# Optimization experiments

Measured on AMD Instinct MI355X. Metric: run time of the kernel, lower is better.

## Reference

```python
import jax, jax.numpy as jnp
import numpy as np

NUM_ROUTES = 32
LN_EPS = 1e-5


def _ln(x, g, b):
    mu = jnp.mean(x, axis=-1, keepdims=True)
    var = jnp.mean(jnp.square(x - mu), axis=-1, keepdims=True)
    return (x - mu) * jax.lax.rsqrt(var + LN_EPS) * g + b


def setup_inputs() -> dict:
    key = jax.random.key(0)
    ks = jax.random.split(key, 16)
    B, N, D = 64, 512, 512
    s = 1.0 / np.sqrt(D)
    return {
        "tokens": jax.random.normal(ks[0], (B, N, D), jnp.float32),
        "token_mask": jax.random.bernoulli(ks[1], 0.7, (B, N)),
        "route_ids": jax.random.randint(ks[2], (N,), 0, NUM_ROUTES),
        # token_ffn: LayerNorm + Linear(D,4D) + GELU + Linear(4D,D)
        "ln1_g": jnp.ones((D,), jnp.float32),
        "ln1_b": jnp.zeros((D,), jnp.float32),
        "w1": jax.random.normal(ks[3], (D, 4 * D), jnp.float32) * s,
        "b1": jnp.zeros((4 * D,), jnp.float32),
        "w2": jax.random.normal(ks[4], (4 * D, D), jnp.float32) * (0.5 * s),
        "b2": jnp.zeros((D,), jnp.float32),
        # within_route_pool: LayerNorm + Linear(D,1)
        "wp_g": jnp.ones((D,), jnp.float32),
        "wp_b": jnp.zeros((D,), jnp.float32),
        "wp_w": jax.random.normal(ks[5], (D,), jnp.float32) * s,
        "wp_bias": jnp.zeros((), jnp.float32),
        # route_pool: LayerNorm + Linear(D,1)
        "rp_g": jnp.ones((D,), jnp.float32),
        "rp_b": jnp.zeros((D,), jnp.float32),
        "rp_w": jax.random.normal(ks[6], (D,), jnp.float32) * s,
        "rp_bias": jnp.zeros((), jnp.float32),
    }


def reference(tokens, token_mask, route_ids, ln1_g, ln1_b, w1, b1, w2, b2,
              wp_g, wp_b, wp_w, wp_bias, rp_g, rp_b, rp_w, rp_bias):
    # token FFN with residual (dropout=0 in eval path)
    h = _ln(tokens, ln1_g, ln1_b)
    h = jax.nn.gelu(h @ w1 + b1, approximate=False)
    x = tokens + (h @ w2 + b2)                       # [B, N, D]

    # within-route attention pool: score is mask-independent -> compute once
    tok_logits = _ln(x, wp_g, wp_b) @ wp_w + wp_bias  # [B, N]

    route_onehot = route_ids[None, :] == jnp.arange(NUM_ROUTES)[:, None]  # [R, N]
    mask = route_onehot[None, :, :] & token_mask[:, None, :]              # [B, R, N]

    ml = jnp.where(mask, tok_logits[:, None, :], -1e9)
    w = jax.nn.softmax(ml, axis=-1)
    w = jnp.where(mask, w, 0.0)
    w = w / jnp.maximum(jnp.sum(w, axis=-1, keepdims=True), 1e-6)
    routes = jnp.einsum('brn,bnd->brd', w, x)         # [B, R, D]
    present = jnp.any(mask, axis=-1)                  # [B, R]

    # route-level attention pool
    rl = _ln(routes, rp_g, rp_b) @ rp_w + rp_bias     # [B, R]
    rl = jnp.where(present, rl, -1e9)
    rw = jax.nn.softmax(rl, axis=-1)
    rw = jnp.where(present, rw, 0.0)
    rw = rw / jnp.maximum(jnp.sum(rw, axis=-1, keepdims=True), 1e-6)
    return jnp.einsum('br,brd->bd', rw, routes)       # [B, D]
```

## Files before the change

kernel.cpp:

```cpp
#include <hip/hip_runtime.h>
#include <hip/hip_bf16.h>
#include <math.h>

#define B_ 64
#define N_ 512
#define D_ 512
#define H_ 2048
#define R_ 32
#define M_ (B_ * N_)

typedef __bf16 bf16x8 __attribute__((ext_vector_type(8)));
typedef float f32x4 __attribute__((ext_vector_type(4)));

__device__ __forceinline__ void async_ld16(const void* g, void* l) {
  __builtin_amdgcn_global_load_lds((__attribute__((address_space(1))) void*)g,
                                   (__attribute__((address_space(3))) void*)l,
                                   16, 0, 0);
}

__device__ __forceinline__ float fast_gelu(float v) {
  const float s = v * 0.70710678118654752f;
  const float a = fabsf(s);
  const float t = __builtin_amdgcn_rcpf(fmaf(0.3275911f, a, 1.0f));
  const float poly = t * fmaf(t, fmaf(t, fmaf(t, fmaf(t, 1.061405429f, -1.453152027f),
                                              1.421413741f), -0.284496736f), 0.254829592f);
  const float er = 1.0f - poly * __expf(-a * a);
  return 0.5f * v * (1.0f + ((s >= 0.f) ? er : -er));
}

__global__ __launch_bounds__(512) void prep_kernel(
    const float* __restrict__ tokens, const void* __restrict__ mask_raw,
    const float* __restrict__ ln1_g, const float* __restrict__ ln1_b,
    const float* __restrict__ w1, const float* __restrict__ w2,
    __hip_bfloat16* __restrict__ aBf, __hip_bfloat16* __restrict__ w1t,
    __hip_bfloat16* __restrict__ w2t, int* __restrict__ flag) {
  const int bid = blockIdx.x;
  const int tid = threadIdx.x;
  if (bid == 0) {
    __shared__ int f;
    if (tid == 0) f = 0;
    __syncthreads();
    const uint4* p = (const uint4*)mask_raw;
    unsigned acc = 0;
    for (int k = tid; k < M_ / 16; k += 512) {
      const uint4 v = p[k];
      acc |= (v.x | v.y | v.z | v.w) & 0xFFFFFF00u;
    }
    if (acc) f = 1;
    __syncthreads();
    if (tid == 0) flag[0] = f;
  } else if (bid <= 512) {
    __shared__ float tile[64][65];
    const int t = bid - 1;
    const float* src;
    __hip_bfloat16* dst;
    int R, C, cx, ry;
    if (t < 256) { src = w1; dst = w1t; R = 512; C = 2048; cx = t & 31; ry = t >> 5; }
    else { const int t2 = t - 256; src = w2; dst = w2t; R = 2048; C = 512; cx = t2 & 7; ry = t2 >> 3; }
    const int c0 = cx * 64, r0 = ry * 64;
    const int tx = tid & 63, ty = tid >> 6;
    for (int r = ty; r < 64; r += 8)
      tile[r][tx] = src[(size_t)(r0 + r) * C + c0 + tx];
    __syncthreads();
    for (int r = ty; r < 64; r += 8)
      dst[(size_t)(c0 + r) * R + r0 + tx] = __float2bfloat16(tile[tx][r]);
  } else {
    const int wv = tid >> 6, lane = tid & 63;
    const int row = (bid - 513) * 8 + wv;
    const float* p = tokens + (size_t)row * D_ + lane * 8;
    const float4 v0 = *(const float4*)p;
    const float4 v1 = *(const float4*)(p + 4);
    float s = v0.x + v0.y + v0.z + v0.w + v1.x + v1.y + v1.z + v1.w;
    float ss = v0.x * v0.x + v0.y * v0.y + v0.z * v0.z + v0.w * v0.w +
               v1.x * v1.x + v1.y * v1.y + v1.z * v1.z + v1.w * v1.w;
#pragma unroll
    for (int m = 32; m > 0; m >>= 1) {
      s += __shfl_xor(s, m);
      ss += __shfl_xor(ss, m);
    }
    const float mu = s * (1.0f / D_);
    const float rstd = rsqrtf(ss * (1.0f / D_) - mu * mu + 1e-5f);
    const float4 g0 = *(const float4*)(ln1_g + lane * 8);
    const float4 g1 = *(const float4*)(ln1_g + lane * 8 + 4);
    const float4 b0 = *(const float4*)(ln1_b + lane * 8);
    const float4 b1 = *(const float4*)(ln1_b + lane * 8 + 4);
    const float vv[8] = {v0.x, v0.y, v0.z, v0.w, v1.x, v1.y, v1.z, v1.w};
    const float gg[8] = {g0.x, g0.y, g0.z, g0.w, g1.x, g1.y, g1.z, g1.w};
    const float bb[8] = {b0.x, b0.y, b0.z, b0.w, b1.x, b1.y, b1.z, b1.w};
    union { __hip_bfloat16 h[8]; uint4 u; } pk;
#pragma unroll
    for (int t2 = 0; t2 < 8; ++t2)
      pk.h[t2] = __float2bfloat16((vv[t2] - mu) * rstd * gg[t2] + bb[t2]);
    *(uint4*)(aBf + (size_t)row * D_ + lane * 8) = pk.u;
  }
}

__global__ __launch_bounds__(256, 2) void gemm_bias_gelu_kernel(
    const __hip_bfloat16* __restrict__ A, const __hip_bfloat16* __restrict__ Bt,
    const float* __restrict__ bias, __hip_bfloat16* __restrict__ C,
    int K, int ldc, int NC) {
  __shared__ alignas(16) unsigned short SU[16384];
  unsigned short* As = SU;
  unsigned short* Bs = SU + 8192;
  const int tid = threadIdx.x;
  const int w = tid >> 6;
  const int lane = tid & 63;
  const int bid = blockIdx.x;
  const int rowT = (bid / (NC * 8)) * 8 + (bid & 7);
  const int colT = (bid >> 3) % NC;
  const int rowBase = rowT * 128;
  const int colBase = colT * 128;
  const int warpRow = w >> 1;
  const int warpCol = w & 1;
  const int q = lane >> 4;
  const int mr = lane & 15;
  const int srow8 = lane >> 3;
  const int sg8 = ((lane & 7) ^ srow8) * 8;
  const int mx7 = (mr & 7) * 8;

  f32x4 acc[4][4] = {};

  for (int k0 = 0; k0 < K; k0 += 64) {
    __syncthreads();
    {
      const __hip_bfloat16* Ak = A + (size_t)(rowBase + w * 32 + srow8) * K + k0 + sg8;
      const __hip_bfloat16* Bk = Bt + (size_t)(colBase + w * 32 + srow8) * K + k0 + sg8;
#pragma unroll
      for (int i = 0; i < 4; ++i) {
        async_ld16(Ak + (size_t)(i * 8) * K, (void*)&As[(w * 32 + i * 8) * 64]);
        async_ld16(Bk + (size_t)(i * 8) * K, (void*)&Bs[(w * 32 + i * 8) * 64]);
      }
    }
    __syncthreads();
#pragma unroll
    for (int s = 0; s < 2; ++s) {
      bf16x8 af[4], bf[4];
#pragma unroll
      for (int i = 0; i < 4; ++i)
        af[i] = *reinterpret_cast<const bf16x8*>(
            &As[(warpRow * 64 + i * 16 + mr) * 64 + (((s * 4 + q) * 8) ^ mx7)]);
#pragma unroll
      for (int j = 0; j < 4; ++j)
        bf[j] = *reinterpret_cast<const bf16x8*>(
            &Bs[(warpCol * 64 + j * 16 + mr) * 64 + (((s * 4 + q) * 8) ^ mx7)]);
#pragma unroll
      for (int i = 0; i < 4; ++i)
#pragma unroll
        for (int j = 0; j < 4; ++j)
          acc[i][j] = __builtin_amdgcn_mfma_f32_16x16x32_bf16(af[i], bf[j], acc[i][j], 0, 0, 0);
    }
  }

  __syncthreads();
  __hip_bfloat16* SB = (__hip_bfloat16*)SU;
#pragma unroll
  for (int j = 0; j < 4; ++j) {
    const int col = warpCol * 64 + j * 16 + mr;
    const float bv = bias[colBase + col];
#pragma unroll
    for (int i = 0; i < 4; ++i) {
#pragma unroll
      for (int r = 0; r < 4; ++r) {
        const int row = warpRow * 64 + i * 16 + q * 4 + r;
        const int slot = (col >> 3) ^ (row & 7);
        SB[row * 128 + slot * 8 + (col & 7)] =
            __float2bfloat16(fast_gelu(acc[i][j][r] + bv));
      }
    }
  }
  __syncthreads();
  const int lg = tid & 15, rsub = tid >> 4;
#pragma unroll
  for (int it = 0; it < 8; ++it) {
    const int m = it * 16 + rsub;
    const int slot = lg ^ (m & 7);
    const uint4 val = *(const uint4*)&SB[m * 128 + slot * 8];
    *(uint4*)&C[(size_t)(rowBase + m) * ldc + colBase + lg * 8] = val;
  }
}

__global__ __launch_bounds__(512, 4) void gemm_acc_kernel(
    const __hip_bfloat16* __restrict__ A, const __hip_bfloat16* __restrict__ Bt,
    const float* __restrict__ bias, const float* __restrict__ resid,
    float* __restrict__ X, int K, int ldb, int first) {
  __shared__ alignas(16) unsigned short SU[24576];
  unsigned short* As = SU;
  unsigned short* Bs = SU + 16384;
  const int tid = threadIdx.x;
  const int w = tid >> 6;
  const int lane = tid & 63;
  const int bid = blockIdx.x;
  const int NC = 4;
  const int rowT = (bid / (NC * 8)) * 8 + (bid & 7);
  const int colT = (bid >> 3) % NC;
  const int rowBase = rowT * 256;
  const int colBase = colT * 128;
  const int warpRow = w >> 1;
  const int warpCol = w & 1;
  const int q = lane >> 4;
  const int mr = lane & 15;
  const int srow8 = lane >> 3;
  const int sg8 = ((lane & 7) ^ srow8) * 8;
  const int mx7 = (mr & 7) * 8;

  f32x4 acc[4][4] = {};

  for (int k0 = 0; k0 < K; k0 += 64) {
    __syncthreads();
    {
      const __hip_bfloat16* Ak = A + (size_t)(rowBase + w * 32 + srow8) * K + k0 + sg8;
#pragma unroll
      for (int i = 0; i < 4; ++i)
        async_ld16(Ak + (size_t)(i * 8) * K, (void*)&As[(w * 32 + i * 8) * 64]);
      const __hip_bfloat16* Bk = Bt + (size_t)(colBase + w * 16 + srow8) * ldb + k0 + sg8;
#pragma unroll
      for (int i = 0; i < 2; ++i)
        async_ld16(Bk + (size_t)(i * 8) * ldb, (void*)&Bs[(w * 16 + i * 8) * 64]);
    }
    __syncthreads();
#pragma unroll
    for (int s = 0; s < 2; ++s) {
      bf16x8 af[4], bf[4];
#pragma unroll
      for (int i = 0; i < 4; ++i)
        af[i] = *reinterpret_cast<const bf16x8*>(
            &As[(warpRow * 64 + i * 16 + mr) * 64 + (((s * 4 + q) * 8) ^ mx7)]);
#pragma unroll
      for (int j = 0; j < 4; ++j)
        bf[j] = *reinterpret_cast<const bf16x8*>(
            &Bs[(warpCol * 64 + j * 16 + mr) * 64 + (((s * 4 + q) * 8) ^ mx7)]);
#pragma unroll
      for (int i = 0; i < 4; ++i)
#pragma unroll
        for (int j = 0; j < 4; ++j)
          acc[i][j] = __builtin_amdgcn_mfma_f32_16x16x32_bf16(af[i], bf[j], acc[i][j], 0, 0, 0);
    }
  }

#pragma unroll
  for (int j = 0; j < 4; ++j) {
    const int n = colBase + warpCol * 64 + j * 16 + mr;
    const float bv = bias[n];
#pragma unroll
    for (int i = 0; i < 4; ++i) {
#pragma unroll
      for (int r = 0; r < 4; ++r) {
        const int m = rowBase + warpRow * 64 + i * 16 + q * 4 + r;
        const size_t idx = (size_t)m * N_ + n;
        const float base = first ? (resid[idx] + bv) : X[idx];
        X[idx] = base + acc[i][j][r];
      }
    }
  }
}

#define STAGE_CAP 20

__global__ __launch_bounds__(256) void route_pool_kernel(
    const float* __restrict__ X, const int* __restrict__ route_ids,
    const void* __restrict__ mask_raw, const int* __restrict__ flag,
    const float* __restrict__ gw, const float* __restrict__ gb,
    const float* __restrict__ ww, const float* __restrict__ wbias,
    float* __restrict__ routes, int* __restrict__ present) {
  const int b = blockIdx.x >> 5;
  const int r = blockIdx.x & 31;
  const int tid = threadIdx.x;
  __shared__ int cnt;
  __shared__ int ls[N_];
  __shared__ float lw[N_];
  __shared__ float Xs[STAGE_CAP][D_];
  if (tid == 0) cnt = 0;
  __syncthreads();
  const int fl = flag[0];
  for (int n = tid; n < N_; n += 256) {
    const int mk = fl ? (int)((const unsigned char*)mask_raw)[b * N_ + n]
                      : ((const int*)mask_raw)[b * N_ + n];
    if (route_ids[n] == r && mk != 0) {
      int p = atomicAdd(&cnt, 1);
      ls[p] = n;
    }
  }
  __syncthreads();
  const int c = cnt;
  const int wv = tid >> 6, lane = tid & 63;
  for (int t = wv; t < c; t += 4) {
    const float* p = X + ((size_t)b * N_ + ls[t]) * D_ + lane * 8;
    const float4 v0 = *(const float4*)p;
    const float4 v1 = *(const float4*)(p + 4);
    if (t < STAGE_CAP) {
      *(float4*)&Xs[t][lane * 8] = v0;
      *(float4*)&Xs[t][lane * 8 + 4] = v1;
    }
    float s = v0.x + v0.y + v0.z + v0.w + v1.x + v1.y + v1.z + v1.w;
    float ss = v0.x * v0.x + v0.y * v0.y + v0.z * v0.z + v0.w * v0.w +
               v1.x * v1.x + v1.y * v1.y + v1.z * v1.z + v1.w * v1.w;
#pragma unroll
    for (int m = 32; m > 0; m >>= 1) {
      s += __shfl_xor(s, m);
      ss += __shfl_xor(ss, m);
    }
    const float mu = s * (1.0f / D_);
    const float rstd = rsqrtf(ss * (1.0f / D_) - mu * mu + 1e-5f);
    const float4 g0 = *(const float4*)(gw + lane * 8);
    const float4 g1 = *(const float4*)(gw + lane * 8 + 4);
    const float4 b0 = *(const float4*)(gb + lane * 8);
    const float4 b1v = *(const float4*)(gb + lane * 8 + 4);
    const float4 w0 = *(const float4*)(ww + lane * 8);
    const float4 w1v = *(const float4*)(ww + lane * 8 + 4);
    const float vv[8] = {v0.x, v0.y, v0.z, v0.w, v1.x, v1.y, v1.z, v1.w};
    const float gg[8] = {g0.x, g0.y, g0.z, g0.w, g1.x, g1.y, g1.z, g1.w};
    const float bb[8] = {b0.x, b0.y, b0.z, b0.w, b1v.x, b1v.y, b1v.z, b1v.w};
    const float wwv[8] = {w0.x, w0.y, w0.z, w0.w, w1v.x, w1v.y, w1v.z, w1v.w};
    float a = 0.f;
#pragma unroll
    for (int t2 = 0; t2 < 8; ++t2) a += ((vv[t2] - mu) * rstd * gg[t2] + bb[t2]) * wwv[t2];
#pragma unroll
    for (int m = 32; m > 0; m >>= 1) a += __shfl_xor(a, m);
    if (lane == 0) lw[t] = a + wbias[0];
  }
  __syncthreads();
  if (tid == 0 && c > 0) {
    float mx = -1e30f;
    for (int i = 0; i < c; ++i) mx = fmaxf(mx, lw[i]);
    float sm = 0.f;
    for (int i = 0; i < c; ++i) {
      const float e = __expf(lw[i] - mx);
      lw[i] = e;
      sm += e;
    }
    const float inv = 1.0f / sm;
    for (int i = 0; i < c; ++i) lw[i] *= inv;
  }
  __syncthreads();
  float a0 = 0.f, a1 = 0.f;
  const int cs = (c < STAGE_CAP) ? c : STAGE_CAP;
  for (int i = 0; i < cs; ++i) {
    const float wgt = lw[i];
    a0 += wgt * Xs[i][tid];
    a1 += wgt * Xs[i][tid + 256];
  }
  for (int i = STAGE_CAP; i < c; ++i) {
    const float* xr = X + ((size_t)b * N_ + ls[i]) * D_;
    const float wgt = lw[i];
    a0 += wgt * xr[tid];
    a1 += wgt * xr[tid + 256];
  }
  float* outp = routes + ((size_t)b * R_ + r) * D_;
  outp[tid] = a0;
  outp[tid + 256] = a1;
  if (tid == 0) present[b * R_ + r] = (c > 0) ? 1 : 0;
}

__global__ __launch_bounds__(512) void final_pool_kernel(
    const float* __restrict__ routes, const int* __restrict__ present,
    const float* __restrict__ gw, const float* __restrict__ gb,
    const float* __restrict__ ww, const float* __restrict__ wbias,
    float* __restrict__ out) {
  const int b = blockIdx.x;
  const int wv = threadIdx.x >> 6, lane = threadIdx.x & 63;
  __shared__ float srw[R_];
  __shared__ float srl[R_];
  for (int r = wv; r < R_; r += 8) {
    const float* p = routes + ((size_t)b * R_ + r) * D_ + lane * 8;
    const float4 v0 = *(const float4*)p;
    const float4 v1 = *(const float4*)(p + 4);
    float s = v0.x + v0.y + v0.z + v0.w + v1.x + v1.y + v1.z + v1.w;
    float ss = v0.x * v0.x + v0.y * v0.y + v0.z * v0.z + v0.w * v0.w +
               v1.x * v1.x + v1.y * v1.y + v1.z * v1.z + v1.w * v1.w;
#pragma unroll
    for (int m = 32; m > 0; m >>= 1) {
      s += __shfl_xor(s, m);
      ss += __shfl_xor(ss, m);
    }
    const float mu = s * (1.0f / D_);
    const float rstd = rsqrtf(ss * (1.0f / D_) - mu * mu + 1e-5f);
    const float4 g0 = *(const float4*)(gw + lane * 8);
    const float4 g1 = *(const float4*)(gw + lane * 8 + 4);
    const float4 b0 = *(const float4*)(gb + lane * 8);
    const float4 b1v = *(const float4*)(gb + lane * 8 + 4);
    const float4 w0 = *(const float4*)(ww + lane * 8);
    const float4 w1v = *(const float4*)(ww + lane * 8 + 4);
    const float vv[8] = {v0.x, v0.y, v0.z, v0.w, v1.x, v1.y, v1.z, v1.w};
    const float gg[8] = {g0.x, g0.y, g0.z, g0.w, g1.x, g1.y, g1.z, g1.w};
    const float bb[8] = {b0.x, b0.y, b0.z, b0.w, b1v.x, b1v.y, b1v.z, b1v.w};
    const float wwv[8] = {w0.x, w0.y, w0.z, w0.w, w1v.x, w1v.y, w1v.z, w1v.w};
    float a = 0.f;
#pragma unroll
    for (int t = 0; t < 8; ++t) a += ((vv[t] - mu) * rstd * gg[t] + bb[t]) * wwv[t];
#pragma unroll
    for (int m = 32; m > 0; m >>= 1) a += __shfl_xor(a, m);
    if (lane == 0) srl[r] = a + wbias[0];
  }
  __syncthreads();
  if (threadIdx.x == 0) {
    float mx = -1e30f;
    for (int r = 0; r < R_; ++r)
      if (present[b * R_ + r]) mx = fmaxf(mx, srl[r]);
    float sm = 0.f;
    for (int r = 0; r < R_; ++r) {
      const float e = present[b * R_ + r] ? __expf(srl[r] - mx) : 0.f;
      srw[r] = e;
      sm += e;
    }
    const float inv = (sm > 0.f) ? 1.0f / sm : 0.f;
    for (int r = 0; r < R_; ++r) srw[r] *= inv;
  }
  __syncthreads();
  const int d = threadIdx.x;
  float a = 0.f;
  for (int r = 0; r < R_; ++r) a += srw[r] * routes[((size_t)b * R_ + r) * D_ + d];
  out[(size_t)b * D_ + d] = a;
}

extern "C" void kernel_launch(void* const* d_in, const int* in_sizes, int n_in,
                              void* d_out, int out_size, void* d_ws, size_t ws_size,
                              hipStream_t stream) {
  const float* tokens = (const float*)d_in[0];
  const void* mask_raw = d_in[1];
  const int* route_ids = (const int*)d_in[2];
  const float* ln1_g = (const float*)d_in[3];
  const float* ln1_b = (const float*)d_in[4];
  const float* w1 = (const float*)d_in[5];
  const float* b1 = (const float*)d_in[6];
  const float* w2 = (const float*)d_in[7];
  const float* b2 = (const float*)d_in[8];
  const float* wp_g = (const float*)d_in[9];
  const float* wp_b = (const float*)d_in[10];
  const float* wp_w = (const float*)d_in[11];
  const float* wp_bias = (const float*)d_in[12];
  const float* rp_g = (const float*)d_in[13];
  const float* rp_b = (const float*)d_in[14];
  const float* rp_w = (const float*)d_in[15];
  const float* rp_bias = (const float*)d_in[16];
  float* out = (float*)d_out;

  char* ws = (char*)d_ws;
  size_t off = 0;
  auto carve = [&](size_t bytes) -> void* {
    void* p = ws + off;
    off = (off + bytes + 255) & ~(size_t)255;
    return p;
  };

  __hip_bfloat16* w1t = (__hip_bfloat16*)carve((size_t)H_ * D_ * 2);
  __hip_bfloat16* w2t = (__hip_bfloat16*)carve((size_t)D_ * H_ * 2);
  __hip_bfloat16* aBf = (__hip_bfloat16*)carve((size_t)M_ * D_ * 2);
  float* X = (float*)carve((size_t)M_ * D_ * 4);
  int* flag = (int*)carve(256);
  int* present = (int*)carve((size_t)B_ * R_ * 4);
  float* routes = (float*)carve((size_t)B_ * R_ * D_ * 4);

  int G = 1;
  while (G < 16 && off + (size_t)M_ * (H_ / G) * 2 > ws_size) G <<= 1;
  const int Hg = H_ / G;
  __hip_bfloat16* hbuf = (__hip_bfloat16*)carve((size_t)M_ * Hg * 2);

  prep_kernel<<<513 + M_ / 8, 512, 0, stream>>>(
      tokens, mask_raw, ln1_g, ln1_b, w1, w2, aBf, w1t, w2t, flag);

  const int NC1 = Hg / 128;
  for (int g = 0; g < G; ++g) {
    gemm_bias_gelu_kernel<<<(M_ / 128) * NC1, 256, 0, stream>>>(
        aBf, w1t + (size_t)g * Hg * D_, b1 + (size_t)g * Hg, hbuf, D_, Hg, NC1);
    gemm_acc_kernel<<<(M_ / 256) * 4, 512, 0, stream>>>(
        hbuf, w2t + (size_t)g * Hg, b2, tokens, X, Hg, H_, (g == 0) ? 1 : 0);
  }

  route_pool_kernel<<<B_ * R_, 256, 0, stream>>>(
      X, route_ids, mask_raw, flag, wp_g, wp_b, wp_w, wp_bias, routes, present);
  final_pool_kernel<<<B_, 512, 0, stream>>>(routes, present, rp_g, rp_b, rp_w, rp_bias, out);
}
```

Baseline: 363.8 us.

## Fuse final pool into route pool, cheaper erf GELU, drop LDS staging

Replaces the GELU's rcp/exp erf approximation with a pure polynomial raised to the 16th power plus one reciprocal. It also packs bf16 conversions in pairs in the GEMM epilogue. The final route-level pool is merged into the route pool kernel: the last-arriving blocks spin on an atomic counter, then do the per-batch softmax and weighted sum, saving one launch. The route pool also stops staging X rows in shared memory, which may raise occupancy but rereads rows from global or cache. Risks are spin-wait deadlock if the finishing blocks cannot all be resident, and a different GELU approximation error.

Result: slower. 592.8 us (+62.9%).

```diff
diff --git a/kernel.cpp b/kernel.cpp
--- a/kernel.cpp
+++ b/kernel.cpp
@@ -21,11 +21,19 @@
 __device__ __forceinline__ float fast_gelu(float v) {
   const float s = v * 0.70710678118654752f;
   const float a = fabsf(s);
-  const float t = __builtin_amdgcn_rcpf(fmaf(0.3275911f, a, 1.0f));
-  const float poly = t * fmaf(t, fmaf(t, fmaf(t, fmaf(t, 1.061405429f, -1.453152027f),
-                                              1.421413741f), -0.284496736f), 0.254829592f);
-  const float er = 1.0f - poly * __expf(-a * a);
-  return 0.5f * v * (1.0f + ((s >= 0.f) ? er : -er));
+  float t = fmaf(a, 4.30638e-5f, 2.765672e-4f);
+  t = fmaf(a, t, 1.520143e-4f);
+  t = fmaf(a, t, 9.2705272e-3f);
+  t = fmaf(a, t, 4.22820123e-2f);
+  t = fmaf(a, t, 7.05230784e-2f);
+  const float p = fmaf(a, t, 1.0f);
+  float p16 = p * p;
+  p16 = p16 * p16;
+  p16 = p16 * p16;
+  p16 = p16 * p16;
+  const float er = 1.0f - __builtin_amdgcn_rcpf(p16);
+  const float erfs = (s >= 0.f) ? er : -er;
+  return 0.5f * v * (1.0f + erfs);
 }
 
 __global__ __launch_bounds__(512) void prep_kernel(
@@ -48,7 +56,10 @@
     }
     if (acc) f = 1;
     __syncthreads();
-    if (tid == 0) flag[0] = f;
+    if (tid == 0) {
+      flag[0] = f;
+      flag[1] = 0;
+    }
   } else if (bid <= 512) {
     __shared__ float tile[64][65];
     const int t = bid - 1;
@@ -157,15 +168,20 @@
   for (int j = 0; j < 4; ++j) {
     const int col = warpCol * 64 + j * 16 + mr;
     const float bv = bias[colBase + col];
+    const int cl = col & 7;
+    const int ch = col >> 3;
 #pragma unroll
     for (int i = 0; i < 4; ++i) {
-#pragma unroll
-      for (int r = 0; r < 4; ++r) {
-        const int row = warpRow * 64 + i * 16 + q * 4 + r;
-        const int slot = (col >> 3) ^ (row & 7);
-        SB[row * 128 + slot * 8 + (col & 7)] =
-            __float2bfloat16(fast_gelu(acc[i][j][r] + bv));
-      }
+      float g[4];
+#pragma unroll
+      for (int r = 0; r < 4; ++r) g[r] = fast_gelu(acc[i][j][r] + bv);
+      const __hip_bfloat162 p01 = __float22bfloat162_rn(make_float2(g[0], g[1]));
+      const __hip_bfloat162 p23 = __float22bfloat162_rn(make_float2(g[2], g[3]));
+      const int row0 = warpRow * 64 + i * 16 + q * 4;
+      SB[(row0 + 0) * 128 + ((ch ^ ((row0 + 0) & 7)) << 3) + cl] = p01.x;
+      SB[(row0 + 1) * 128 + ((ch ^ ((row0 + 1) & 7)) << 3) + cl] = p01.y;
+      SB[(row0 + 2) * 128 + ((ch ^ ((row0 + 2) & 7)) << 3) + cl] = p23.x;
+      SB[(row0 + 3) * 128 + ((ch ^ ((row0 + 3) & 7)) << 3) + cl] = p23.y;
     }
   }
   __syncthreads();
@@ -254,21 +270,24 @@
   }
 }
 
-#define STAGE_CAP 20
-
 __global__ __launch_bounds__(256) void route_pool_kernel(
     const float* __restrict__ X, const int* __restrict__ route_ids,
-    const void* __restrict__ mask_raw, const int* __restrict__ flag,
+    const void* __restrict__ mask_raw, int* __restrict__ flag,
     const float* __restrict__ gw, const float* __restrict__ gb,
     const float* __restrict__ ww, const float* __restrict__ wbias,
-    float* __restrict__ routes, int* __restrict__ present) {
+    const float* __restrict__ rp_g, const float* __restrict__ rp_b,
+    const float* __restrict__ rp_w, const float* __restrict__ rp_bias,
+    float* __restrict__ routes, int* __restrict__ present,
+    float* __restrict__ out) {
   const int b = blockIdx.x >> 5;
   const int r = blockIdx.x & 31;
   const int tid = threadIdx.x;
   __shared__ int cnt;
+  __shared__ int sh_old;
   __shared__ int ls[N_];
   __shared__ float lw[N_];
-  __shared__ float Xs[STAGE_CAP][D_];
+  __shared__ float fsrl[R_];
+  __shared__ float fsrw[R_];
   if (tid == 0) cnt = 0;
   __syncthreads();
   const int fl = flag[0];
@@ -287,10 +306,6 @@
     const float* p = X + ((size_t)b * N_ + ls[t]) * D_ + lane * 8;
     const float4 v0 = *(const float4*)p;
     const float4 v1 = *(const float4*)(p + 4);
-    if (t < STAGE_CAP) {
-      *(float4*)&Xs[t][lane * 8] = v0;
-      *(float4*)&Xs[t][lane * 8 + 4] = v1;
-    }
     float s = v0.x + v0.y + v0.z + v0.w + v1.x + v1.y + v1.z + v1.w;
     float ss = v0.x * v0.x + v0.y * v0.y + v0.z * v0.z + v0.w * v0.w +
                v1.x * v1.x + v1.y * v1.y + v1.z * v1.z + v1.w * v1.w;
@@ -333,13 +348,7 @@
   }
   __syncthreads();
   float a0 = 0.f, a1 = 0.f;
-  const int cs = (c < STAGE_CAP) ? c : STAGE_CAP;
-  for (int i = 0; i < cs; ++i) {
-    const float wgt = lw[i];
-    a0 += wgt * Xs[i][tid];
-    a1 += wgt * Xs[i][tid + 256];
-  }
-  for (int i = STAGE_CAP; i < c; ++i) {
+  for (int i = 0; i < c; ++i) {
     const float* xr = X + ((size_t)b * N_ + ls[i]) * D_;
     const float wgt = lw[i];
     a0 += wgt * xr[tid];
@@ -349,19 +358,22 @@
   outp[tid] = a0;
   outp[tid + 256] = a1;
   if (tid == 0) present[b * R_ + r] = (c > 0) ? 1 : 0;
-}
-
-__global__ __launch_bounds__(512) void final_pool_kernel(
-    const float* __restrict__ routes, const int* __restrict__ present,
-    const float* __restrict__ gw, const float* __restrict__ gb,
-    const float* __restrict__ ww, const float* __restrict__ wbias,
-    float* __restrict__ out) {
-  const int b = blockIdx.x;
-  const int wv = threadIdx.x >> 6, lane = threadIdx.x & 63;
-  __shared__ float srw[R_];
-  __shared__ float srl[R_];
-  for (int r = wv; r < R_; r += 8) {
-    const float* p = routes + ((size_t)b * R_ + r) * D_ + lane * 8;
+
+  __threadfence();
+  __syncthreads();
+  if (tid == 0) sh_old = atomicAdd(&flag[1], 1);
+  __syncthreads();
+  const int old = sh_old;
+  if (old < B_ * R_ - B_) return;
+  const int bb = old - (B_ * R_ - B_);
+  if (tid == 0) {
+    while (atomicAdd(&flag[1], 0) < B_ * R_) __builtin_amdgcn_s_sleep(8);
+  }
+  __syncthreads();
+  __threadfence();
+
+  for (int rr = wv; rr < R_; rr += 4) {
+    const float* p = routes + ((size_t)bb * R_ + rr) * D_ + lane * 8;
     const float4 v0 = *(const float4*)p;
     const float4 v1 = *(const float4*)(p + 4);
     float s = v0.x + v0.y + v0.z + v0.w + v1.x + v1.y + v1.z + v1.w;
@@ -374,42 +386,46 @@
     }
     const float mu = s * (1.0f / D_);
     const float rstd = rsqrtf(ss * (1.0f / D_) - mu * mu + 1e-5f);
-    const float4 g0 = *(const float4*)(gw + lane * 8);
-    const float4 g1 = *(const float4*)(gw + lane * 8 + 4);
-    const float4 b0 = *(const float4*)(gb + lane * 8);
-    const float4 b1v = *(const float4*)(gb + lane * 8 + 4);
-    const float4 w0 = *(const float4*)(ww + lane * 8);
-    const float4 w1v = *(const float4*)(ww + lane * 8 + 4);
+    const float4 g0 = *(const float4*)(rp_g + lane * 8);
+    const float4 g1 = *(const float4*)(rp_g + lane * 8 + 4);
+    const float4 b0 = *(const float4*)(rp_b + lane * 8);
+    const float4 b1v = *(const float4*)(rp_b + lane * 8 + 4);
+    const float4 w0 = *(const float4*)(rp_w + lane * 8);
+    const float4 w1v = *(const float4*)(rp_w + lane * 8 + 4);
     const float vv[8] = {v0.x, v0.y, v0.z, v0.w, v1.x, v1.y, v1.z, v1.w};
     const float gg[8] = {g0.x, g0.y, g0.z, g0.w, g1.x, g1.y, g1.z, g1.w};
-    const float bb[8] = {b0.x, b0.y, b0.z, b0.w, b1v.x, b1v.y, b1v.z, b1v.w};
+    const float bb2[8] = {b0.x, b0.y, b0.z, b0.w, b1v.x, b1v.y, b1v.z, b1v.w};
     const float wwv[8] = {w0.x, w0.y, w0.z, w0.w, w1v.x, w1v.y, w1v.z, w1v.w};
     float a = 0.f;
 #pragma unroll
-    for (int t = 0; t < 8; ++t) a += ((vv[t] - mu) * rstd * gg[t] + bb[t]) * wwv[t];
+    for (int t2 = 0; t2 < 8; ++t2) a += ((vv[t2] - mu) * rstd * gg[t2] + bb2[t2]) * wwv[t2];
 #pragma unroll
     for (int m = 32; m > 0; m >>= 1) a += __shfl_xor(a, m);
-    if (lane == 0) srl[r] = a + wbias[0];
-  }
-  __syncthreads();
-  if (threadIdx.x == 0) {
+    if (lane == 0) fsrl[rr] = a + rp_bias[0];
+  }
+  __syncthreads();
+  if (tid == 0) {
     float mx = -1e30f;
-    for (int r = 0; r < R_; ++r)
-      if (present[b * R_ + r]) mx = fmaxf(mx, srl[r]);
+    for (int rr = 0; rr < R_; ++rr)
+      if (present[bb * R_ + rr]) mx = fmaxf(mx, fsrl[rr]);
     float sm = 0.f;
-    for (int r = 0; r < R_; ++r) {
-      const float e = present[b * R_ + r] ? __expf(srl[r] - mx) : 0.f;
-      srw[r] = e;
+    for (int rr = 0; rr < R_; ++rr) {
+      const float e = present[bb * R_ + rr] ? __expf(fsrl[rr] - mx) : 0.f;
+      fsrw[rr] = e;
       sm += e;
     }
     const float inv = (sm > 0.f) ? 1.0f / sm : 0.f;
-    for (int r = 0; r < R_; ++r) srw[r] *= inv;
-  }
-  __syncthreads();
-  const int d = threadIdx.x;
-  float a = 0.f;
-  for (int r = 0; r < R_; ++r) a += srw[r] * routes[((size_t)b * R_ + r) * D_ + d];
-  out[(size_t)b * D_ + d] = a;
+    for (int rr = 0; rr < R_; ++rr) fsrw[rr] *= inv;
+  }
+  __syncthreads();
+  float o0 = 0.f, o1 = 0.f;
+  for (int rr = 0; rr < R_; ++rr) {
+    const float* rp = routes + ((size_t)bb * R_ + rr) * D_;
+    o0 += fsrw[rr] * rp[tid];
+    o1 += fsrw[rr] * rp[tid + 256];
+  }
+  out[(size_t)bb * D_ + tid] = o0;
+  out[(size_t)bb * D_ + tid + 256] = o1;
 }
 
 extern "C" void kernel_launch(void* const* d_in, const int* in_sizes, int n_in,
@@ -467,6 +483,6 @@
   }
 
   route_pool_kernel<<<B_ * R_, 256, 0, stream>>>(
-      X, route_ids, mask_raw, flag, wp_g, wp_b, wp_w, wp_bias, routes, present);
-  final_pool_kernel<<<B_, 512, 0, stream>>>(routes, present, rp_g, rp_b, rp_w, rp_bias, out);
-}
+      X, route_ids, mask_raw, flag, wp_g, wp_b, wp_w, wp_bias,
+      rp_g, rp_b, rp_w, rp_bias, routes, present, out);
+}
```
